# Kernel optimization log

Hardware: AMD Instinct MI355X
Metric: run time of the kernel (lower is better)

Reference implementation:

```python
import jax, jax.numpy as jnp
import numpy as np

VEC = 90  # per-anchor vector length: obj(1)+box(4)+1 unused? -> layout: [p, dx, dy, dw, dh, _, 12 point, 72 seg]


def _decode(out, thresh, t, anchors, case):
    """Dense, mask-based version of Detector._filter + Detector._parse.

    The torch code gathers rows via nonzero (data-dependent shape); for a
    jit-compatible reference we decode every cell and zero out rows whose
    sigmoid(objectness) <= thresh. Row layout matches torch exactly:
    [n, sigmoid(p), cx, cy, w, h, point(12), seg(72)].
    """
    B, C, H, W = out.shape
    v = jnp.transpose(out, (0, 2, 3, 1)).reshape(B, H, W, 3, VEC)
    p = v[..., 0]
    mask = jax.nn.sigmoid(p) > thresh                      # [B,H,W,3]
    iy = jnp.arange(H, dtype=v.dtype)[None, :, None, None]
    ix = jnp.arange(W, dtype=v.dtype)[None, None, :, None]
    cy = (iy + v[..., 2]) * t
    cx = (ix + v[..., 1]) * t
    w = anchors[:, 0] * jnp.exp(v[..., 3])                 # broadcast over anchor dim
    h = anchors[:, 1] * jnp.exp(v[..., 4])
    s = jnp.sqrt(w * w + h * h) / case                     # diagonal / case, [B,H,W,3]
    point = v[..., 6:18] * s[..., None]                    # 6 (x,y) keypoint pairs scaled
    seg = v[..., 18:90].reshape(B, H, W, 3, 24, 3)         # 24 triplets (coord, sig, sig)
    seg = jnp.concatenate(
        [seg[..., :1] * s[..., None, None], jax.nn.sigmoid(seg[..., 1:3])],
        axis=-1).reshape(B, H, W, 3, 72)
    n = jnp.broadcast_to(jnp.arange(B, dtype=v.dtype)[:, None, None, None], p.shape)
    obj = jnp.stack([n, jax.nn.sigmoid(p), cx, cy, w, h], axis=-1)
    rows = jnp.concatenate([obj, point, seg], axis=-1).reshape(-1, VEC)
    return jnp.where(mask.reshape(-1, 1), rows, jnp.zeros((), rows.dtype))


def setup_inputs() -> dict:
    key = jax.random.key(0)
    ks = jax.random.split(key, 7)
    B = 32
    return {
        "out13": jax.random.normal(ks[0], (B, 270, 13, 13), jnp.float32),
        "out26": jax.random.normal(ks[1], (B, 270, 26, 26), jnp.float32),
        "out52": jax.random.normal(ks[2], (B, 270, 52, 52), jnp.float32),
        "anchors13": jax.random.uniform(ks[3], (3, 2), jnp.float32, 50.0, 300.0),
        "anchors26": jax.random.uniform(ks[4], (3, 2), jnp.float32, 20.0, 120.0),
        "anchors52": jax.random.uniform(ks[5], (3, 2), jnp.float32, 5.0, 60.0),
        "thresh": jax.random.uniform(ks[6], (1,), jnp.float32, 0.4, 0.7),
        "case": 416,
    }


def reference(out13, out26, out52, anchors13, anchors26, anchors52, thresh, case):
    th = thresh[0]
    c = jnp.float32(case)
    boxes = jnp.concatenate([
        _decode(out13, th, jnp.float32(32.0), anchors13, c),
        _decode(out26, th, jnp.float32(16.0), anchors26, c),
        _decode(out52, th, jnp.float32(8.0), anchors52, c),
    ], axis=0)
    return boxes
```

## Files before the change

### kernel.cpp

```cpp
#include <hip/hip_runtime.h>
#include <math.h>

#define PX 32
#define NT 192
#define HPX 16
#define LROWS (HPX * 3)

__device__ __forceinline__ float sigf(float x) { return 1.0f / (1.0f + expf(-x)); }

template<bool F4>
__device__ __forceinline__ void flushLds(const float* __restrict__ lds,
                                         float* __restrict__ outp, int nfl, int tid)
{
    if (F4) {
        float4* d4 = (float4*)outp;
        const float4* s4 = (const float4*)lds;
        for (int i = tid; i < (nfl >> 2); i += NT) d4[i] = s4[i];
        int rem = nfl & 3, tail = nfl & ~3;
        if (tid < rem) outp[tail + tid] = lds[tail + tid];
    } else {
        float2* d2 = (float2*)outp;
        const float2* s2 = (const float2*)lds;
        for (int i = tid; i < (nfl >> 1); i += NT) d2[i] = s2[i];
    }
}

template<int H, int W, int T, bool F4>
__device__ __forceinline__ void decode_level(
    const float* __restrict__ in, const float* __restrict__ anchors,
    float th, float invCase, float* __restrict__ out, long gRowBase,
    int blkL, float* __restrict__ lds)
{
    constexpr int HW = H * W;
    constexpr int SPANS = (HW + PX - 1) / PX;
    const int b    = blkL / SPANS;
    const int P0   = (blkL % SPANS) * PX;
    const int npix = (HW - P0 < PX) ? (HW - P0) : PX;

    const int tid  = threadIdx.x;
    const int a    = tid >> 6;
    const int lane = tid & 63;
    const int h    = lane >> 5;
    const int p    = lane & 31;
    const bool act = (p < npix);

    float v[45];
    if (act) {
        const int pix = P0 + p;
        const int x   = pix % W;
        const int y   = pix / W;
        const float* src = in + ((long)b * 270 + a * 90 + 45 * h) * HW + pix;

        #pragma unroll
        for (int j = 0; j < 45; ++j) v[j] = src[(long)j * HW];

        float sp = sigf(v[0]);
        bool  m  = sp > th;
        float A0 = anchors[a * 2 + 0], A1 = anchors[a * 2 + 1];
        float w  = A0 * expf(v[3]);
        float hb = A1 * expf(v[4]);
        float s  = sqrtf(w * w + hb * hb) * invCase;
        float cx = ((float)x + v[1]) * (float)T;
        float cy = ((float)y + v[2]) * (float)T;

        float ms = __shfl(m ? s : 0.0f, p, 64);
        float mf = __shfl(m ? 1.0f : 0.0f, p, 64);
        const bool mB = mf > 0.5f;

        #pragma unroll
        for (int j = 0; j < 45; ++j) {
            float val = v[j];
            bool coordAlways = (j % 3 == 0);
            bool pointRegion = (j >= 6 && j < 18);
            if (coordAlways)      v[j] = val * ms;
            else if (pointRegion) v[j] = (h == 0) ? val * ms : (mB ? sigf(val) : 0.0f);
            else                  v[j] = mB ? sigf(val) : 0.0f;
        }
        if (h == 0) {
            v[0] = m ? (float)b : 0.0f;
            v[1] = m ? sp       : 0.0f;
            v[2] = m ? cx       : 0.0f;
            v[3] = m ? cy       : 0.0f;
            v[4] = m ? w        : 0.0f;
            v[5] = m ? hb       : 0.0f;
        }
    }

    const size_t gbase = (size_t)(gRowBase + ((long)b * HW + P0) * 3) * 90;

    if (act && p < HPX) {
        float* dst = lds + (p * 3 + a) * 90 + 45 * h;
        #pragma unroll
        for (int j = 0; j < 45; ++j) dst[j] = v[j];
    }
    __syncthreads();
    int npixA = npix < HPX ? npix : HPX;
    flushLds<F4>(lds, out + gbase, npixA * 3 * 90, tid);

    int npixB = npix - HPX;
    if (npixB > 0) {
        __syncthreads();
        if (act && p >= HPX) {
            float* dst = lds + ((p - HPX) * 3 + a) * 90 + 45 * h;
            #pragma unroll
            for (int j = 0; j < 45; ++j) dst[j] = v[j];
        }
        __syncthreads();
        flushLds<F4>(lds, out + gbase + (size_t)LROWS * 90, npixB * 3 * 90, tid);
    }
}

__global__ __launch_bounds__(NT, 6) void decode_all(
    const float* __restrict__ in13, const float* __restrict__ in26,
    const float* __restrict__ in52,
    const float* __restrict__ anc13, const float* __restrict__ anc26,
    const float* __restrict__ anc52,
    const float* __restrict__ thresh, const int* __restrict__ casep,
    float* __restrict__ out, int nblk52, int nblk26, long rows13, long rows26)
{
    __shared__ float lds[LROWS * 90];
    const float th = thresh[0];
    const float invCase = 1.0f / (float)(*casep);
    const int blk = blockIdx.x;

    if (blk < nblk52)
        decode_level<52, 52, 8, true>(in52, anc52, th, invCase, out,
                                      rows13 + rows26, blk, lds);
    else if (blk < nblk52 + nblk26)
        decode_level<26, 26, 16, true>(in26, anc26, th, invCase, out,
                                       rows13, blk - nblk52, lds);
    else
        decode_level<13, 13, 32, false>(in13, anc13, th, invCase, out,
                                        0, blk - nblk52 - nblk26, lds);
}

extern "C" void kernel_launch(void* const* d_in, const int* in_sizes, int n_in,
                              void* d_out, int out_size, void* d_ws, size_t ws_size,
                              hipStream_t stream) {
    const float* in13  = (const float*)d_in[0];
    const float* in26  = (const float*)d_in[1];
    const float* in52  = (const float*)d_in[2];
    const float* anc13 = (const float*)d_in[3];
    const float* anc26 = (const float*)d_in[4];
    const float* anc52 = (const float*)d_in[5];
    const float* th    = (const float*)d_in[6];
    const int*   casep = (const int*)d_in[7];
    float* out = (float*)d_out;

    int B = in_sizes[0] / (270 * 13 * 13);

    long rows13 = (long)B * 13 * 13 * 3;
    long rows26 = (long)B * 26 * 26 * 3;

    int nblk13 = B * ((13 * 13 + PX - 1) / PX);
    int nblk26 = B * ((26 * 26 + PX - 1) / PX);
    int nblk52 = B * ((52 * 52 + PX - 1) / PX);

    decode_all<<<dim3(nblk52 + nblk26 + nblk13), dim3(NT), 0, stream>>>(
        in13, in26, in52, anc13, anc26, anc52, th, casep, out,
        nblk52, nblk26, rows13, rows26);
}
```

Before: 54.52 us.

## Stage input tile through LDS with float4 loads and single-pass output flush

Input channels for each 32-pixel span are loaded cooperatively into LDS with float4 global loads, replacing the strided per-thread scalar loads. Threads then read their 45 values from LDS. The LDS buffer grows to the full 270x32 tile, so all 32 pixels are written and flushed in one pass instead of two half-passes. The larger shared footprint lowers the launch-bounds occupancy hint from 6 to 3 and adds one extra barrier.

After: 69.01 us. 1.27x slower.

```diff
diff --git a/kernel.cpp b/kernel.cpp
--- a/kernel.cpp
+++ b/kernel.cpp
@@ -3,29 +3,11 @@
 
 #define PX 32
 #define NT 192
-#define HPX 16
-#define LROWS (HPX * 3)
+#define RAWF (270 * PX)
 
 __device__ __forceinline__ float sigf(float x) { return 1.0f / (1.0f + expf(-x)); }
 
-template<bool F4>
-__device__ __forceinline__ void flushLds(const float* __restrict__ lds,
-                                         float* __restrict__ outp, int nfl, int tid)
-{
-    if (F4) {
-        float4* d4 = (float4*)outp;
-        const float4* s4 = (const float4*)lds;
-        for (int i = tid; i < (nfl >> 2); i += NT) d4[i] = s4[i];
-        int rem = nfl & 3, tail = nfl & ~3;
-        if (tid < rem) outp[tail + tid] = lds[tail + tid];
-    } else {
-        float2* d2 = (float2*)outp;
-        const float2* s2 = (const float2*)lds;
-        for (int i = tid; i < (nfl >> 1); i += NT) d2[i] = s2[i];
-    }
-}
-
-template<int H, int W, int T, bool F4>
+template<int H, int W, int T, bool VEC>
 __device__ __forceinline__ void decode_level(
     const float* __restrict__ in, const float* __restrict__ anchors,
     float th, float invCase, float* __restrict__ out, long gRowBase,
@@ -36,23 +18,44 @@
     const int b    = blkL / SPANS;
     const int P0   = (blkL % SPANS) * PX;
     const int npix = (HW - P0 < PX) ? (HW - P0) : PX;
+    const int tid  = threadIdx.x;
 
-    const int tid  = threadIdx.x;
-    const int a    = tid >> 6;
-    const int lane = tid & 63;
-    const int h    = lane >> 5;
-    const int p    = lane & 31;
-    const bool act = (p < npix);
+    const float* srcb = in + (long)b * (270LL * HW) + P0;
 
+    if (VEC) {
+        #pragma unroll
+        for (int k = 0; k < 11; ++k) {
+            int i = tid + k * NT;
+            int part = i & 7, ch = i >> 3;
+            if (part * 4 < npix) {
+                float4 val = *(const float4*)(srcb + (long)ch * HW + part * 4);
+                *(float4*)(&lds[i * 4]) = val;
+            }
+        }
+        {   int i = tid + 11 * NT;
+            if (i < RAWF / 4) {
+                int part = i & 7, ch = i >> 3;
+                if (part * 4 < npix) {
+                    float4 val = *(const float4*)(srcb + (long)ch * HW + part * 4);
+                    *(float4*)(&lds[i * 4]) = val;
+                }
+            }
+        }
+    } else {
+        for (int i = tid; i < RAWF; i += NT) {
+            int p = i & (PX - 1), ch = i >> 5;
+            if (p < npix) lds[i] = srcb[(long)ch * HW + p];
+        }
+    }
+    __syncthreads();
+
+    const int a = tid >> 6, lane = tid & 63, h = lane >> 5, p = lane & 31;
+    const bool act = p < npix;
     float v[45];
     if (act) {
-        const int pix = P0 + p;
-        const int x   = pix % W;
-        const int y   = pix / W;
-        const float* src = in + ((long)b * 270 + a * 90 + 45 * h) * HW + pix;
-
+        const float* rs = lds + (a * 90 + 45 * h) * PX + p;
         #pragma unroll
-        for (int j = 0; j < 45; ++j) v[j] = src[(long)j * HW];
+        for (int j = 0; j < 45; ++j) v[j] = rs[j * PX];
 
         float sp = sigf(v[0]);
         bool  m  = sp > th;
@@ -60,6 +63,8 @@
         float w  = A0 * expf(v[3]);
         float hb = A1 * expf(v[4]);
         float s  = sqrtf(w * w + hb * hb) * invCase;
+        int pix = P0 + p;
+        int x = pix % W, y = pix / W;
         float cx = ((float)x + v[1]) * (float)T;
         float cy = ((float)y + v[2]) * (float)T;
 
@@ -85,32 +90,29 @@
             v[5] = m ? hb       : 0.0f;
         }
     }
+    __syncthreads();
 
-    const size_t gbase = (size_t)(gRowBase + ((long)b * HW + P0) * 3) * 90;
-
-    if (act && p < HPX) {
+    if (act) {
         float* dst = lds + (p * 3 + a) * 90 + 45 * h;
         #pragma unroll
         for (int j = 0; j < 45; ++j) dst[j] = v[j];
     }
     __syncthreads();
-    int npixA = npix < HPX ? npix : HPX;
-    flushLds<F4>(lds, out + gbase, npixA * 3 * 90, tid);
 
-    int npixB = npix - HPX;
-    if (npixB > 0) {
-        __syncthreads();
-        if (act && p >= HPX) {
-            float* dst = lds + ((p - HPX) * 3 + a) * 90 + 45 * h;
-            #pragma unroll
-            for (int j = 0; j < 45; ++j) dst[j] = v[j];
-        }
-        __syncthreads();
-        flushLds<F4>(lds, out + gbase + (size_t)LROWS * 90, npixB * 3 * 90, tid);
+    const int nfl = npix * 3 * 90;
+    const size_t gbase = (size_t)(gRowBase + ((long)b * HW + P0) * 3) * 90;
+    if (VEC) {
+        float4* d4 = (float4*)(out + gbase);
+        const float4* s4 = (const float4*)lds;
+        for (int i = tid; i < (nfl >> 2); i += NT) d4[i] = s4[i];
+    } else {
+        float2* d2 = (float2*)(out + gbase);
+        const float2* s2 = (const float2*)lds;
+        for (int i = tid; i < (nfl >> 1); i += NT) d2[i] = s2[i];
     }
 }
 
-__global__ __launch_bounds__(NT, 6) void decode_all(
+__global__ __launch_bounds__(NT, 3) void decode_all(
     const float* __restrict__ in13, const float* __restrict__ in26,
     const float* __restrict__ in52,
     const float* __restrict__ anc13, const float* __restrict__ anc26,
@@ -118,7 +120,7 @@
     const float* __restrict__ thresh, const int* __restrict__ casep,
     float* __restrict__ out, int nblk52, int nblk26, long rows13, long rows26)
 {
-    __shared__ float lds[LROWS * 90];
+    __shared__ float lds[RAWF];
     const float th = thresh[0];
     const float invCase = 1.0f / (float)(*casep);
     const int blk = blockIdx.x;
```

## Process two pixels per thread with vectorized loads and nontemporal stores

Applied to the files above, without the earlier changes.

For the 52 and 26 levels, each thread now handles two adjacent pixels, so its input reads become float2 loads and each block covers 64 pixels, flushed through LDS in four 16-pixel chunks. All output flushes now use nontemporal stores. Launch bounds drop from 6 to 4 waves to make room for the doubled register use. The aim is fewer, wider memory transactions and less cache pollution from the large output write, at the cost of extra register pressure and more barriers per block.

After: 54.92 us. Within noise of the previous version (+0.7%).

```diff
diff --git a/kernel.cpp b/kernel.cpp
--- a/kernel.cpp
+++ b/kernel.cpp
@@ -1,56 +1,140 @@
 #include <hip/hip_runtime.h>
 #include <math.h>
 
-#define PX 32
-#define NT 192
-#define HPX 16
-#define LROWS (HPX * 3)
+#define NT  192
+#define PXW 64
+#define PXS 32
+#define FR  48
+
+typedef float vf4 __attribute__((ext_vector_type(4)));
+typedef float vf2 __attribute__((ext_vector_type(2)));
 
 __device__ __forceinline__ float sigf(float x) { return 1.0f / (1.0f + expf(-x)); }
 
-template<bool F4>
-__device__ __forceinline__ void flushLds(const float* __restrict__ lds,
+__device__ __forceinline__ void ntflush4(const float* __restrict__ lds,
                                          float* __restrict__ outp, int nfl, int tid)
 {
-    if (F4) {
-        float4* d4 = (float4*)outp;
-        const float4* s4 = (const float4*)lds;
-        for (int i = tid; i < (nfl >> 2); i += NT) d4[i] = s4[i];
-        int rem = nfl & 3, tail = nfl & ~3;
-        if (tid < rem) outp[tail + tid] = lds[tail + tid];
-    } else {
-        float2* d2 = (float2*)outp;
-        const float2* s2 = (const float2*)lds;
-        for (int i = tid; i < (nfl >> 1); i += NT) d2[i] = s2[i];
-    }
-}
-
-template<int H, int W, int T, bool F4>
-__device__ __forceinline__ void decode_level(
+    vf4* d4 = (vf4*)outp;
+    const vf4* s4 = (const vf4*)lds;
+    for (int i = tid; i < (nfl >> 2); i += NT)
+        __builtin_nontemporal_store(s4[i], d4 + i);
+}
+__device__ __forceinline__ void ntflush2(const float* __restrict__ lds,
+                                         float* __restrict__ outp, int nfl, int tid)
+{
+    vf2* d2 = (vf2*)outp;
+    const vf2* s2 = (const vf2*)lds;
+    for (int i = tid; i < (nfl >> 1); i += NT)
+        __builtin_nontemporal_store(s2[i], d2 + i);
+}
+
+template<int H, int W, int T>
+__device__ __forceinline__ void decode_wide(
     const float* __restrict__ in, const float* __restrict__ anchors,
     float th, float invCase, float* __restrict__ out, long gRowBase,
     int blkL, float* __restrict__ lds)
 {
     constexpr int HW = H * W;
-    constexpr int SPANS = (HW + PX - 1) / PX;
+    constexpr int SPANS = (HW + PXW - 1) / PXW;
     const int b    = blkL / SPANS;
-    const int P0   = (blkL % SPANS) * PX;
-    const int npix = (HW - P0 < PX) ? (HW - P0) : PX;
-
-    const int tid  = threadIdx.x;
-    const int a    = tid >> 6;
-    const int lane = tid & 63;
-    const int h    = lane >> 5;
-    const int p    = lane & 31;
-    const bool act = (p < npix);
+    const int P0   = (blkL % SPANS) * PXW;
+    const int npix = (HW - P0 < PXW) ? (HW - P0) : PXW;
+
+    const int tid = threadIdx.x;
+    const int a = tid >> 6, lane = tid & 63, h = lane >> 5, p2 = lane & 31;
+    const int q0 = 2 * p2;
+    const bool act = q0 < npix;
+
+    float v0[45], v1[45];
+    if (act) {
+        const float* src = in + ((long)b * 270 + a * 90 + 45 * h) * HW + P0 + q0;
+        #pragma unroll
+        for (int j = 0; j < 45; ++j) {
+            vf2 t2 = *(const vf2*)(src + (long)j * HW);
+            v0[j] = t2.x; v1[j] = t2.y;
+        }
+
+        float sp0 = sigf(v0[0]), sp1 = sigf(v1[0]);
+        bool  m0 = sp0 > th,     m1 = sp1 > th;
+        float A0 = anchors[a * 2 + 0], A1 = anchors[a * 2 + 1];
+        float w0 = A0 * expf(v0[3]), w1 = A0 * expf(v1[3]);
+        float h0 = A1 * expf(v0[4]), h1 = A1 * expf(v1[4]);
+        float s0 = sqrtf(w0 * w0 + h0 * h0) * invCase;
+        float s1 = sqrtf(w1 * w1 + h1 * h1) * invCase;
+        int pix0 = P0 + q0;
+        int x0 = pix0 % W, y0 = pix0 / W;
+        int x1 = (pix0 + 1) % W, y1 = (pix0 + 1) / W;
+        float cx0 = ((float)x0 + v0[1]) * (float)T, cy0 = ((float)y0 + v0[2]) * (float)T;
+        float cx1 = ((float)x1 + v1[1]) * (float)T, cy1 = ((float)y1 + v1[2]) * (float)T;
+
+        float ms0 = __shfl(m0 ? s0 : 0.0f, p2, 64);
+        float ms1 = __shfl(m1 ? s1 : 0.0f, p2, 64);
+        float mf0 = __shfl(m0 ? 1.0f : 0.0f, p2, 64);
+        float mf1 = __shfl(m1 ? 1.0f : 0.0f, p2, 64);
+        const bool mB0 = mf0 > 0.5f, mB1 = mf1 > 0.5f;
+
+        #pragma unroll
+        for (int j = 0; j < 45; ++j) {
+            bool coord = (j % 3 == 0), pt = (j >= 6 && j < 18);
+            float a0 = v0[j], a1 = v1[j];
+            if (coord)   { v0[j] = a0 * ms0;  v1[j] = a1 * ms1; }
+            else if (pt) { v0[j] = (h == 0) ? a0 * ms0 : (mB0 ? sigf(a0) : 0.0f);
+                           v1[j] = (h == 0) ? a1 * ms1 : (mB1 ? sigf(a1) : 0.0f); }
+            else         { v0[j] = mB0 ? sigf(a0) : 0.0f;
+                           v1[j] = mB1 ? sigf(a1) : 0.0f; }
+        }
+        if (h == 0) {
+            v0[0] = m0 ? (float)b : 0.0f;  v1[0] = m1 ? (float)b : 0.0f;
+            v0[1] = m0 ? sp0 : 0.0f;       v1[1] = m1 ? sp1 : 0.0f;
+            v0[2] = m0 ? cx0 : 0.0f;       v1[2] = m1 ? cx1 : 0.0f;
+            v0[3] = m0 ? cy0 : 0.0f;       v1[3] = m1 ? cy1 : 0.0f;
+            v0[4] = m0 ? w0  : 0.0f;       v1[4] = m1 ? w1  : 0.0f;
+            v0[5] = m0 ? h0  : 0.0f;       v1[5] = m1 ? h1  : 0.0f;
+        }
+    }
+
+    const size_t gbase = (size_t)(gRowBase + ((long)b * HW + P0) * 3) * 90;
+    const int myf = p2 >> 3;
+
+    #pragma unroll
+    for (int f = 0; f < PXW / 16; ++f) {
+        int pf = npix - 16 * f;
+        if (pf <= 0) break;
+        if (pf > 16) pf = 16;
+        if (act && myf == f) {
+            float* dst = lds + ((q0 - 16 * f) * 3 + a) * 90 + 45 * h;
+            #pragma unroll
+            for (int j = 0; j < 45; ++j) dst[j] = v0[j];
+            dst += 270;
+            #pragma unroll
+            for (int j = 0; j < 45; ++j) dst[j] = v1[j];
+        }
+        __syncthreads();
+        ntflush4(lds, out + gbase + (size_t)f * FR * 90, pf * 3 * 90, tid);
+        __syncthreads();
+    }
+}
+
+__device__ __forceinline__ void decode13(
+    const float* __restrict__ in, const float* __restrict__ anchors,
+    float th, float invCase, float* __restrict__ out,
+    int blkL, float* __restrict__ lds)
+{
+    constexpr int H = 13, W = 13, T = 32, HW = 169;
+    constexpr int SPANS = (HW + PXS - 1) / PXS;
+    const int b    = blkL / SPANS;
+    const int P0   = (blkL % SPANS) * PXS;
+    const int npix = (HW - P0 < PXS) ? (HW - P0) : PXS;
+
+    const int tid = threadIdx.x;
+    const int a = tid >> 6, lane = tid & 63, h = lane >> 5, p = lane & 31;
+    const bool act = p < npix;
 
     float v[45];
     if (act) {
         const int pix = P0 + p;
-        const int x   = pix % W;
-        const int y   = pix / W;
+        const int x = pix % W, y = pix / W;
         const float* src = in + ((long)b * 270 + a * 90 + 45 * h) * HW + pix;
-
         #pragma unroll
         for (int j = 0; j < 45; ++j) v[j] = src[(long)j * HW];
 
@@ -70,11 +154,10 @@
         #pragma unroll
         for (int j = 0; j < 45; ++j) {
             float val = v[j];
-            bool coordAlways = (j % 3 == 0);
-            bool pointRegion = (j >= 6 && j < 18);
-            if (coordAlways)      v[j] = val * ms;
-            else if (pointRegion) v[j] = (h == 0) ? val * ms : (mB ? sigf(val) : 0.0f);
-            else                  v[j] = mB ? sigf(val) : 0.0f;
+            bool coord = (j % 3 == 0), pt = (j >= 6 && j < 18);
+            if (coord)   v[j] = val * ms;
+            else if (pt) v[j] = (h == 0) ? val * ms : (mB ? sigf(val) : 0.0f);
+            else         v[j] = mB ? sigf(val) : 0.0f;
         }
         if (h == 0) {
             v[0] = m ? (float)b : 0.0f;
@@ -86,31 +169,31 @@
         }
     }
 
-    const size_t gbase = (size_t)(gRowBase + ((long)b * HW + P0) * 3) * 90;
-
-    if (act && p < HPX) {
+    const size_t gbase = (size_t)(((long)b * HW + P0) * 3) * 90;
+
+    if (act && p < 16) {
         float* dst = lds + (p * 3 + a) * 90 + 45 * h;
         #pragma unroll
         for (int j = 0; j < 45; ++j) dst[j] = v[j];
     }
     __syncthreads();
-    int npixA = npix < HPX ? npix : HPX;
-    flushLds<F4>(lds, out + gbase, npixA * 3 * 90, tid);
-
-    int npixB = npix - HPX;
-    if (npixB > 0) {
-        __syncthreads();
-        if (act && p >= HPX) {
-            float* dst = lds + ((p - HPX) * 3 + a) * 90 + 45 * h;
+    int nA = npix < 16 ? npix : 16;
+    ntflush2(lds, out + gbase, nA * 3 * 90, tid);
+
+    int nB = npix - 16;
+    if (nB > 0) {
+        __syncthreads();
+        if (act && p >= 16) {
+            float* dst = lds + ((p - 16) * 3 + a) * 90 + 45 * h;
             #pragma unroll
             for (int j = 0; j < 45; ++j) dst[j] = v[j];
         }
         __syncthreads();
-        flushLds<F4>(lds, out + gbase + (size_t)LROWS * 90, npixB * 3 * 90, tid);
-    }
-}
-
-__global__ __launch_bounds__(NT, 6) void decode_all(
+        ntflush2(lds, out + gbase + (size_t)FR * 90, nB * 3 * 90, tid);
+    }
+}
+
+__global__ __launch_bounds__(NT, 4) void decode_all(
     const float* __restrict__ in13, const float* __restrict__ in26,
     const float* __restrict__ in52,
     const float* __restrict__ anc13, const float* __restrict__ anc26,
@@ -118,20 +201,19 @@
     const float* __restrict__ thresh, const int* __restrict__ casep,
     float* __restrict__ out, int nblk52, int nblk26, long rows13, long rows26)
 {
-    __shared__ float lds[LROWS * 90];
+    __shared__ float lds[FR * 90];
     const float th = thresh[0];
     const float invCase = 1.0f / (float)(*casep);
     const int blk = blockIdx.x;
 
     if (blk < nblk52)
-        decode_level<52, 52, 8, true>(in52, anc52, th, invCase, out,
-                                      rows13 + rows26, blk, lds);
+        decode_wide<52, 52, 8>(in52, anc52, th, invCase, out,
+                               rows13 + rows26, blk, lds);
     else if (blk < nblk52 + nblk26)
-        decode_level<26, 26, 16, true>(in26, anc26, th, invCase, out,
-                                       rows13, blk - nblk52, lds);
+        decode_wide<26, 26, 16>(in26, anc26, th, invCase, out,
+                                rows13, blk - nblk52, lds);
     else
-        decode_level<13, 13, 32, false>(in13, anc13, th, invCase, out,
-                                        0, blk - nblk52 - nblk26, lds);
+        decode13(in13, anc13, th, invCase, out, blk - nblk52 - nblk26, lds);
 }
 
 extern "C" void kernel_launch(void* const* d_in, const int* in_sizes, int n_in,
@@ -152,9 +234,9 @@
     long rows13 = (long)B * 13 * 13 * 3;
     long rows26 = (long)B * 26 * 26 * 3;
 
-    int nblk13 = B * ((13 * 13 + PX - 1) / PX);
-    int nblk26 = B * ((26 * 26 + PX - 1) / PX);
-    int nblk52 = B * ((52 * 52 + PX - 1) / PX);
+    int nblk13 = B * ((13 * 13 + PXS - 1) / PXS);
+    int nblk26 = B * ((26 * 26 + PXW - 1) / PXW);
+    int nblk52 = B * ((52 * 52 + PXW - 1) / PXW);
 
     decode_all<<<dim3(nblk52 + nblk26 + nblk13), dim3(NT), 0, stream>>>(
         in13, in26, in52, anc13, anc26, anc52, th, casep, out,
```
